# Kernel tuning notes

Hardware: AMD Instinct MI355X
Metric: run time of the kernel (lower is better)

Reference implementation:

```python
import jax, jax.numpy as jnp
import numpy as np

S, B, C, H, W = 16, 64, 128, 11, 11
P = H * W
N_ITER = 3
EPS = 1e-5


def setup_inputs() -> dict:
    key = jax.random.key(0)
    ks = jax.random.split(key, 12)
    w = lambda k, shape: jax.random.normal(k, shape, jnp.float32) * 0.02
    return {
        "x": jax.random.normal(ks[0], (S, B, C, H, W), jnp.float32),
        # intra-attention 1x1 convs (stored as [out,in] matrices)
        "wq": w(ks[1], (C, C)), "bq": jnp.zeros((C,), jnp.float32),
        "wk": w(ks[2], (C, C)), "bk": jnp.zeros((C,), jnp.float32),
        "wv": w(ks[3], (C, C)), "bv": jnp.zeros((C,), jnp.float32),
        "intra_alpha": jnp.float32(1.0),
        # inter-message path
        "w_msg": w(ks[4], (C, C + 1)), "b_msg": jnp.zeros((C,), jnp.float32),
        "w_lin": w(ks[5], (C, C)),
        "weight": jnp.float32(0.5),
        "w_gate": w(ks[6], (C, C)), "b_gate": jnp.zeros((C,), jnp.float32),
        # ConvGRU 3x3 convs
        "w_zr": w(ks[7], (2 * C, 2 * C, 3, 3)), "b_zr": jnp.zeros((2 * C,), jnp.float32),
        "w_h": w(ks[8], (C, 2 * C, 3, 3)), "b_h": jnp.zeros((C,), jnp.float32),
        # LayerNorm over [C,11,11]
        "ln_gamma": jnp.ones((C, H, W), jnp.float32),
        "ln_beta": jnp.zeros((C, H, W), jnp.float32),
    }


def reference(x, wq, bq, wk, bk, wv, bv, intra_alpha, w_msg, b_msg, w_lin,
              weight, w_gate, b_gate, w_zr, b_zr, w_h, b_h, ln_gamma, ln_beta):
    scale = C ** -0.5

    def c1(t, wgt, bias):  # 1x1 conv on [S,B,Cin,H,W] -> [S,B,Cout,H,W]
        return jnp.einsum('sbchw,oc->sbohw', t, wgt) + bias[:, None, None]

    def conv3(t, wgt, bias):  # 3x3 'SAME' conv on [N,Cin,H,W]
        y = jax.lax.conv_general_dilated(
            t, wgt, (1, 1), 'SAME', dimension_numbers=('NCHW', 'OIHW', 'NCHW'))
        return y + bias[None, :, None, None]

    # chain-graph neighbor validity masks (|i-j| == 1)
    mask_l = (jnp.arange(S) >= 1).astype(x.dtype)[:, None, None, None, None]
    mask_r = (jnp.arange(S) <= S - 2).astype(x.dtype)[:, None, None, None, None]

    h = x
    for _ in range(N_ITER):
        # ---- intra spatial self-attention (per node, over P=H*W tokens) ----
        q = c1(h, wq, bq).reshape(S, B, C, P)
        k = c1(h, wk, bk).reshape(S, B, C, P)
        v = c1(h, wv, bv).reshape(S, B, C, P)
        att = jax.nn.softmax(jnp.einsum('sbcp,sbcq->sbpq', q, k) * scale, axis=-1)
        intra = jnp.einsum('sbpq,sbcq->sbcp', att, v).reshape(S, B, C, H, W)
        intra = intra_alpha * intra + h

        # ---- inter gated message attention from chain neighbors ----
        xf = h.reshape(S, B, C, P)

        def gated_msg(y, edge_val):
            ef = jnp.full((S, B, 1, H, W), edge_val, h.dtype)  # edge feature i-j
            yy = c1(jnp.concatenate([y, ef], axis=2), w_msg, b_msg).reshape(S, B, C, P)
            yy = jnp.einsum('sbcp,dc->sbdp', yy, w_lin)  # Linear (no bias)
            a = jax.nn.softmax(jnp.einsum('sbcp,sbcq->sbpq', xf, yy), axis=-1)
            m = jnp.einsum('sbpq,sbcq->sbcp', a, yy).reshape(S, B, C, H, W)
            g = jax.nn.sigmoid(c1(m, w_gate, b_gate).mean(axis=(-2, -1), keepdims=True))
            return m * g

        y_left = jnp.concatenate([jnp.zeros_like(h[:1]), h[:-1]], axis=0)   # h[i-1], edge +1
        y_right = jnp.concatenate([h[1:], jnp.zeros_like(h[:1])], axis=0)   # h[i+1], edge -1
        inter = gated_msg(y_left, 1.0) * mask_l + gated_msg(y_right, -1.0) * mask_r

        comb = weight * intra + (1.0 - weight) * inter

        # ---- ConvGRU update (fold S into batch) ----
        xg = comb.reshape(S * B, C, H, W)
        hg = h.reshape(S * B, C, H, W)
        zr = jax.nn.sigmoid(conv3(jnp.concatenate([xg, hg], axis=1), w_zr, b_zr))
        z, r = zr[:, :C], zr[:, C:]
        h_hat = jnp.tanh(conv3(jnp.concatenate([xg, r * hg], axis=1), w_h, b_h))
        h_new = ((1 - z) * hg + z * h_hat).reshape(S, B, C, H, W)

        # ---- residual + LayerNorm over [C,H,W] ----
        nh = h_new + h
        mu = nh.mean(axis=(-3, -2, -1), keepdims=True)
        var = nh.var(axis=(-3, -2, -1), keepdims=True)
        h = (nh - mu) * jax.lax.rsqrt(var + EPS) * ln_gamma + ln_beta
    return h
```

## Files before the change

### kernel.cpp

```cpp
#include <hip/hip_runtime.h>
#include <hip/hip_bf16.h>

#define S_   16
#define B_   64
#define SBn  1024
#define C_   128
#define P_   121
#define CP_  15488
static const long NEl = 15859712L;

typedef __hip_bfloat16 bf16t;
typedef __attribute__((ext_vector_type(8))) short bf16x8;
typedef __attribute__((ext_vector_type(4))) float f32x4;
typedef __attribute__((ext_vector_type(4))) unsigned short us4;

__device__ __forceinline__ float ldb(const bf16t* p){ return __bfloat162float(*p); }
__device__ __forceinline__ float b2f(unsigned short u){ unsigned x=((unsigned)u)<<16; float f; __builtin_memcpy(&f,&x,4); return f; }
__device__ __forceinline__ unsigned short f2bu(float v){ __hip_bfloat16 b=__float2bfloat16(v); unsigned short u; __builtin_memcpy(&u,&b,2); return u; }
__device__ __forceinline__ float ldin(const void* s, long i, int f){
    return f ? ((const float*)s)[i] : b2f(((const unsigned short*)s)[i]);
}

__global__ void detect_kernel(const unsigned short* __restrict__ x, int* __restrict__ flag){
    if(blockIdx.x==0 && threadIdx.x==0){
        int crazy=0;
        for(int i=0;i<512;i++){
            unsigned e=(x[i]>>7)&0xFF;
            if(e!=0 && (e<64 || e>191)) crazy++;
        }
        *flag=(crazy>40)?1:0;
    }
}

__global__ void cvt_kernel(float* __restrict__ dst, const void* __restrict__ src, long n, const int* __restrict__ flag){
    long i=(long)blockIdx.x*blockDim.x+threadIdx.x;
    long st=(long)gridDim.x*blockDim.x;
    int f=*flag;
    for(;i<n;i+=st) dst[i]=ldin(src,i,f);
}

__global__ __launch_bounds__(256) void cvtT_kernel(bf16t* __restrict__ hT, const void* __restrict__ x, const int* __restrict__ flag){
    __shared__ bf16t tl[CP_];
    int sb=blockIdx.x, t=threadIdx.x; int f=*flag;
    for(int i=t;i<CP_;i+=256)
        tl[i]=__float2bfloat16(ldin(x,(long)sb*CP_+i,f));
    __syncthreads();
    bf16t* ho=hT+(size_t)sb*CP_;
    for(int j=t;j<CP_;j+=256){
        int p=j>>7, c=j&127;
        ho[j]=tl[c*P_+p];
    }
}

__global__ __launch_bounds__(128) void prep_msg_kernel(float* __restrict__ W2, float* __restrict__ b2l, float* __restrict__ b2r,
        const void* __restrict__ wlin, const void* __restrict__ wmsg, const void* __restrict__ bmsg, const int* __restrict__ flag){
    int d=blockIdx.x, c=threadIdx.x; int f=*flag;
    float acc=0.f;
    for(int o2=0;o2<C_;o2++) acc += ldin(wlin,(long)d*C_+o2,f)*ldin(wmsg,(long)o2*(C_+1)+c,f);
    W2[d*C_+c]=acc;
    if(c<2){
        float e=(c==0)?1.f:-1.f; float a=0.f;
        for(int o2=0;o2<C_;o2++) a += ldin(wlin,(long)d*C_+o2,f)*(ldin(bmsg,o2,f)+e*ldin(wmsg,(long)o2*(C_+1)+C_,f));
        if(c==0) b2l[d]=a; else b2r[d]=a;
    }
}

template<int RAW>
__global__ void prep_w1t(bf16t* __restrict__ dst, const void* __restrict__ src, const int* __restrict__ flag){
    int idx=blockIdx.x*blockDim.x+threadIdx.x;
    if(idx>=16384) return;
    int r=idx&31, oc=(idx>>5)&127, icb=idx>>12;
    float v = RAW? ldin(src,(long)oc*C_+icb*32+r,*flag) : ((const float*)src)[(long)oc*C_+icb*32+r];
    dst[idx]=__float2bfloat16(v);
}

__global__ void prep_w3t(bf16t* __restrict__ dst, const void* __restrict__ src, const int* __restrict__ flag, int OC){
    int idx=blockIdx.x*blockDim.x+threadIdx.x;
    int tot=OC*2304;
    if(idx>=tot) return;
    int r=idx&31; int rest=idx>>5; int oc=rest%OC; int g2=rest/OC; int icb=g2&7, tap=g2>>3;
    float v=ldin(src,((long)(oc*256+icb*32+r))*9+tap,*flag);
    dst[idx]=__float2bfloat16(v);
}

__global__ void prep_gbt(float* __restrict__ gamT, float* __restrict__ betT,
                         const void* __restrict__ gam, const void* __restrict__ bet, const int* __restrict__ flag){
    int idx=blockIdx.x*blockDim.x+threadIdx.x;
    if(idx>=CP_) return;
    int c=idx/P_, p=idx-c*P_; int f=*flag;
    gamT[p*C_+c]=ldin(gam,idx,f);
    betT[p*C_+c]=ldin(bet,idx,f);
}

__global__ void prep_wgt(float* __restrict__ wgT, float* __restrict__ bg2,
                         const void* __restrict__ wg, const void* __restrict__ bg, const int* __restrict__ flag){
    int idx=blockIdx.x*blockDim.x+threadIdx.x;
    int f=*flag;
    if(idx<16384){ int k=idx>>7, c=idx&127; wgT[idx]=ldin(wg,(long)c*C_+k,f); }
    if(idx<128) bg2[idx]=ldin(bg,idx,f);
}

__device__ __forceinline__ void gemm24r(f32x4 (&acc)[4][2],
    const bf16t* __restrict__ Wt, const bf16x8 (&hreg)[4][2],
    int ocr,int l15,int kg)
{
    #pragma unroll
    for(int i=0;i<4;i++){
        #pragma unroll
        for(int j=0;j<2;j++) acc[i][j]=(f32x4){0.f,0.f,0.f,0.f};
    }
    #pragma unroll
    for(int kc=0;kc<4;kc++){
        bf16x8 a[4];
        #pragma unroll
        for(int mt=0;mt<4;mt++) a[mt]=*(const bf16x8*)(Wt+((size_t)(kc*C_+ocr*64+mt*16+l15))*32+kg*8);
        #pragma unroll
        for(int mt=0;mt<4;mt++){
            #pragma unroll
            for(int nt=0;nt<2;nt++)
                acc[mt][nt]=__builtin_amdgcn_mfma_f32_16x16x32_bf16(a[mt],hreg[kc][nt],acc[mt][nt],0,0,0);
        }
    }
}

__device__ __forceinline__ void msg_phase(
    f32x4 (&res)[8], const bf16t* __restrict__ hT, int sb, int shift,
    const bf16t* __restrict__ W2T, const float* __restrict__ b2e,
    const float* __restrict__ wgT, const float* __restrict__ bgf, float w1m,
    const bf16x8 (&areg)[4],
    bf16t* LA, bf16t* LB, float* fl,
    int t,int w,int l15,int kg,int ocr,int pcr)
{
    __syncthreads();
    const bf16t* hsp=hT+(size_t)(sb+shift)*CP_;
    bf16x8 hregS[4][2];
    #pragma unroll
    for(int kc=0;kc<4;kc++){
        #pragma unroll
        for(int nt=0;nt<2;nt++)
            hregS[kc][nt]=*(const bf16x8*)(hsp+(size_t)(pcr*32+nt*16+l15)*C_+kc*32+kg*8);
    }
    f32x4 acc[4][2];
    gemm24r(acc,W2T,hregS,ocr,l15,kg);
    #pragma unroll
    for(int mt=0;mt<4;mt++){
        int oc0=ocr*64+mt*16+kg*4;
        #pragma unroll
        for(int nt=0;nt<2;nt++){
            int p=pcr*32+nt*16+l15;
            us4 pk;
            #pragma unroll
            for(int r=0;r<4;r++){
                float v=acc[mt][nt][r]+b2e[oc0+r];
                pk[r]=f2bu(v);
                LB[(oc0+r)*136+p]=__float2bfloat16(p<P_? v : 0.f);
            }
            *(us4*)(LA+p*136+oc0)=pk;
        }
    }
    __syncthreads();
    int m0=w*16;
    f32x4 s[8];
    #pragma unroll
    for(int nt=0;nt<8;nt++) s[nt]=(f32x4){0.f,0.f,0.f,0.f};
    #pragma unroll
    for(int kc=0;kc<4;kc++){
        #pragma unroll
        for(int nt=0;nt<8;nt++){
            bf16x8 b=*(const bf16x8*)(LA+(size_t)(nt*16+l15)*136+kc*32+kg*8);
            s[nt]=__builtin_amdgcn_mfma_f32_16x16x32_bf16(areg[kc],b,s[nt],0,0,0);
        }
    }
    if(l15>=9){
        #pragma unroll
        for(int r=0;r<4;r++) s[7][r]=-3.0e38f;
    }
    #pragma unroll
    for(int r=0;r<4;r++){
        float mx=s[0][r];
        #pragma unroll
        for(int nt=1;nt<8;nt++) mx=fmaxf(mx,s[nt][r]);
        #pragma unroll
        for(int o=1;o<16;o<<=1) mx=fmaxf(mx,__shfl_xor(mx,o));
        float sm=0.f;
        #pragma unroll
        for(int nt=0;nt<8;nt++){ float e=__expf(s[nt][r]-mx); s[nt][r]=e; sm+=e; }
        #pragma unroll
        for(int o=1;o<16;o<<=1) sm+=__shfl_xor(sm,o);
        float rs=1.f/sm;
        #pragma unroll
        for(int nt=0;nt<8;nt++) s[nt][r]*=rs;
    }
    __syncthreads();
    #pragma unroll
    for(int r=0;r<4;r++){
        int pr=m0+kg*4+r;
        #pragma unroll
        for(int nt=0;nt<8;nt++) LA[pr*136+nt*16+l15]=__float2bfloat16(s[nt][r]);
    }
    __syncthreads();
    f32x4 o[8];
    #pragma unroll
    for(int nt=0;nt<8;nt++) o[nt]=(f32x4){0.f,0.f,0.f,0.f};
    #pragma unroll
    for(int jc=0;jc<4;jc++){
        bf16x8 a=*(const bf16x8*)(LB+(size_t)(m0+l15)*136+jc*32+kg*8);
        #pragma unroll
        for(int nt=0;nt<8;nt++){
            bf16x8 b=*(const bf16x8*)(LA+(size_t)(nt*16+l15)*136+jc*32+kg*8);
            o[nt]=__builtin_amdgcn_mfma_f32_16x16x32_bf16(a,b,o[nt],0,0,0);
        }
    }
    int c0=m0+kg*4;
    #pragma unroll
    for(int r=0;r<4;r++){
        float sm=0.f;
        #pragma unroll
        for(int nt=0;nt<8;nt++){ float v=o[nt][r]; if(nt==7&&l15>8) v=0.f; sm+=v; }
        sm+=__shfl_xor(sm,1); sm+=__shfl_xor(sm,2); sm+=__shfl_xor(sm,4); sm+=__shfl_xor(sm,8);
        if(l15==0) fl[c0+r]=sm*(1.f/121.f);
    }
    __syncthreads();
    if(t<C_){
        float a=bgf[t];
        #pragma unroll 8
        for(int k=0;k<C_;k++) a+=wgT[k*C_+t]*fl[k];
        fl[C_+t]=1.f/(1.f+__expf(-a));
    }
    __syncthreads();
    float gg[4];
    #pragma unroll
    for(int r=0;r<4;r++) gg[r]=fl[C_+c0+r];
    #pragma unroll
    for(int nt=0;nt<8;nt++){
        #pragma unroll
        for(int r=0;r<4;r++) res[nt][r]+=w1m*o[nt][r]*gg[r];
    }
}

__global__ __launch_bounds__(512) void attn_all(
    bf16t* __restrict__ comb, const bf16t* __restrict__ hT,
    const bf16t* __restrict__ WqT, const bf16t* __restrict__ WkT, const bf16t* __restrict__ WvT,
    const float* __restrict__ bq, const float* __restrict__ bk, const float* __restrict__ bv,
    const bf16t* __restrict__ W2T, const float* __restrict__ b2l, const float* __restrict__ b2r,
    const float* __restrict__ wgT, const float* __restrict__ bgf,
    const float* __restrict__ alphap, const float* __restrict__ wp)
{
    __shared__ bf16t LA[128*136];
    __shared__ bf16t LB[128*136];
    __shared__ float fl[256];
    int sb=blockIdx.x, t=threadIdx.x, lane=t&63, w=t>>6;
    int l15=lane&15, kg=lane>>4;
    const bf16t* hp=hT+(size_t)sb*CP_;
    int ocr=w>>2, pcr=w&3;
    int m0=w*16;
    bf16x8 hreg[4][2];
    #pragma unroll
    for(int kc=0;kc<4;kc++){
        #pragma unroll
        for(int nt=0;nt<2;nt++)
            hreg[kc][nt]=*(const bf16x8*)(hp+(size_t)(pcr*32+nt*16+l15)*C_+kc*32+kg*8);
    }
    bf16x8 areg[4];
    #pragma unroll
    for(int kc=0;kc<4;kc++)
        areg[kc]=*(const bf16x8*)(hp+(size_t)(m0+l15)*C_+kc*32+kg*8);

    f32x4 acc[4][2];
    gemm24r(acc,WqT,hreg,ocr,l15,kg);
    #pragma unroll
    for(int mt=0;mt<4;mt++){
        int oc0=ocr*64+mt*16+kg*4;
        #pragma unroll
        for(int nt=0;nt<2;nt++){
            int p=pcr*32+nt*16+l15;
            us4 pk;
            #pragma unroll
            for(int r=0;r<4;r++) pk[r]=f2bu(acc[mt][nt][r]+bq[oc0+r]);
            *(us4*)(LA+p*136+oc0)=pk;
        }
    }
    gemm24r(acc,WkT,hreg,ocr,l15,kg);
    #pragma unroll
    for(int mt=0;mt<4;mt++){
        int oc0=ocr*64+mt*16+kg*4;
        #pragma unroll
        for(int nt=0;nt<2;nt++){
            int p=pcr*32+nt*16+l15;
            us4 pk;
            #pragma unroll
            for(int r=0;r<4;r++) pk[r]=f2bu(acc[mt][nt][r]+bk[oc0+r]);
            *(us4*)(LB+p*136+oc0)=pk;
        }
    }
    __syncthreads();
    f32x4 s[8];
    #pragma unroll
    for(int nt=0;nt<8;nt++) s[nt]=(f32x4){0.f,0.f,0.f,0.f};
    #pragma unroll
    for(int kc=0;kc<4;kc++){
        bf16x8 a=*(const bf16x8*)(LA+(size_t)(m0+l15)*136+kc*32+kg*8);
        #pragma unroll
        for(int nt=0;nt<8;nt++){
            bf16x8 b=*(const bf16x8*)(LB+(size_t)(nt*16+l15)*136+kc*32+kg*8);
            s[nt]=__builtin_amdgcn_mfma_f32_16x16x32_bf16(a,b,s[nt],0,0,0);
        }
    }
    const float scale=0.08838834764831845f;
    #pragma unroll
    for(int nt=0;nt<8;nt++){
        #pragma unroll
        for(int r=0;r<4;r++) s[nt][r]*=scale;
    }
    if(l15>=9){
        #pragma unroll
        for(int r=0;r<4;r++) s[7][r]=-3.0e38f;
    }
    #pragma unroll
    for(int r=0;r<4;r++){
        float mx=s[0][r];
        #pragma unroll
        for(int nt=1;nt<8;nt++) mx=fmaxf(mx,s[nt][r]);
        #pragma unroll
        for(int o=1;o<16;o<<=1) mx=fmaxf(mx,__shfl_xor(mx,o));
        float sm=0.f;
        #pragma unroll
        for(int nt=0;nt<8;nt++){ float e=__expf(s[nt][r]-mx); s[nt][r]=e; sm+=e; }
        #pragma unroll
        for(int o=1;o<16;o<<=1) sm+=__shfl_xor(sm,o);
        float rs=1.f/sm;
        #pragma unroll
        for(int nt=0;nt<8;nt++) s[nt][r]*=rs;
    }
    __syncthreads();
    gemm24r(acc,WvT,hreg,ocr,l15,kg);
    #pragma unroll
    for(int mt=0;mt<4;mt++){
        int oc0=ocr*64+mt*16+kg*4;
        #pragma unroll
        for(int nt=0;nt<2;nt++){
            int p=pcr*32+nt*16+l15;
            #pragma unroll
            for(int r=0;r<4;r++)
                LA[(oc0+r)*136+p]=__float2bfloat16(p<P_? acc[mt][nt][r]+bv[oc0+r] : 0.f);
        }
    }
    #pragma unroll
    for(int r=0;r<4;r++){
        int pr=m0+kg*4+r;
        #pragma unroll
        for(int nt=0;nt<8;nt++) LB[pr*136+nt*16+l15]=__float2bfloat16(s[nt][r]);
    }
    __syncthreads();
    f32x4 res[8];
    #pragma unroll
    for(int nt=0;nt<8;nt++) res[nt]=(f32x4){0.f,0.f,0.f,0.f};
    #pragma unroll
    for(int jc=0;jc<4;jc++){
        bf16x8 a=*(const bf16x8*)(LA+(size_t)(m0+l15)*136+jc*32+kg*8);
        #pragma unroll
        for(int nt=0;nt<8;nt++){
            bf16x8 b=*(const bf16x8*)(LB+(size_t)(nt*16+l15)*136+jc*32+kg*8);
            res[nt]=__builtin_amdgcn_mfma_f32_16x16x32_bf16(a,b,res[nt],0,0,0);
        }
    }
    float al=*alphap, wv=*wp, w1m=1.f-wv;
    int c0=m0+kg*4;
    #pragma unroll
    for(int nt=0;nt<8;nt++){
        int p=nt*16+l15;
        int pc=(p<P_)?p:(P_-1);
        us4 hv=*(const us4*)(hp+(size_t)pc*C_+c0);
        #pragma unroll
        for(int r=0;r<4;r++) res[nt][r]=wv*(al*res[nt][r]+b2f(hv[r]));
    }
    if(sb>=B_)
        msg_phase(res,hT,sb,-B_,W2T,b2l,wgT,bgf,w1m,areg,LA,LB,fl,t,w,l15,kg,ocr,pcr);
    if(sb<SBn-B_)
        msg_phase(res,hT,sb, B_,W2T,b2r,wgT,bgf,w1m,areg,LA,LB,fl,t,w,l15,kg,ocr,pcr);
    __syncthreads();
    unsigned short* tl=(unsigned short*)LA;
    #pragma unroll
    for(int nt=0;nt<8;nt++){
        int p=nt*16+l15;
        if(p>=P_) continue;
        us4 pk;
        #pragma unroll
        for(int r=0;r<4;r++) pk[r]=f2bu(res[nt][r]);
        *(us4*)(tl+p*C_+c0)=pk;
    }
    __syncthreads();
    bf16t* ob=comb+(size_t)sb*CP_;
    for(int j=t;j<1936;j+=512)
        *(bf16x8*)(ob+j*8)=*(const bf16x8*)(tl+j*8);
}

#define LOADA3(bidx, widx) { \
    _Pragma("unroll") \
    for(int mt=0;mt<4;mt++) abuf[bidx][mt]=*(const bf16x8*)(Wt+(size_t)(widx)*(OC*32)+mt*512+base_lane); }
#define STEP3(lbase, bidx, doff) { \
    bf16x8 bb[4]; \
    _Pragma("unroll") \
    for(int nt=0;nt<4;nt++) bb[nt]=*(const bf16x8*)((lbase)+boff[nt]+(doff)); \
    __builtin_amdgcn_s_setprio(1); \
    _Pragma("unroll") \
    for(int mt=0;mt<4;mt++){ \
        _Pragma("unroll") \
        for(int nt=0;nt<4;nt++) \
            acc[mt][nt]=__builtin_amdgcn_mfma_f32_16x16x32_bf16(abuf[bidx][mt],bb[nt],acc[mt][nt],0,0,0); } \
    __builtin_amdgcn_s_setprio(0); }

#define SLOADZ(stg) { \
    const bf16t* ssrc=(((stg)<2)? in0T:in1T)+(size_t)sb*CP_+((stg)&1)*64; \
    sreg[0]=*(const bf16x8*)(ssrc+(size_t)sp0*C_+(t&7)*8); \
    if(sv1) sreg[1]=*(const bf16x8*)(ssrc+(size_t)sp1*C_+(t&7)*8); }
#define SWRITEZ(lbase) { \
    *(bf16x8*)((lbase)+spix0*72+(t&7)*8)=sreg[0]; \
    if(sv1) *(bf16x8*)((lbase)+spix1*72+(t&7)*8)=sreg[1]; }

__global__ __launch_bounds__(512) void conv3_zr(
    bf16t* __restrict__ o0, bf16t* __restrict__ o1,
    const bf16t* __restrict__ in0T, const bf16t* __restrict__ in1T,
    const bf16t* __restrict__ Wt, const float* __restrict__ bias,
    const bf16t* __restrict__ hTb)
{
    constexpr int OC=256;
    __shared__ bf16t lin[2*12176];
    int sb=blockIdx.x;
    int t=threadIdx.x, lane=t&63, w=t>>6;
    int ocb=(w>=4)?128:0; int w2=w&3;
    int ocr=w2>>1, pcr=w2&1, l15=lane&15, kg=lane>>4;
    int boff[4]; bool pv_[4];
    #pragma unroll
    for(int nt=0;nt<4;nt++){
        int p=pcr*64+nt*16+l15;
        pv_[nt]=(p<P_); int pc=pv_[nt]?p:(P_-1);
        boff[nt]=((pc/11)*13+(pc%11))*72+kg*8;
    }
    f32x4 acc[4][4];
    #pragma unroll
    for(int i=0;i<4;i++){
        #pragma unroll
        for(int j=0;j<4;j++) acc[i][j]=(f32x4){0.f,0.f,0.f,0.f};
    }
    int base_lane=(ocb+ocr*64+l15)*32+kg*8;
    bf16x8 abuf[4][4];
    bf16x8 sreg[2];
    bool sv1=((t+512)<968);
    int sp0=t>>3, sp1=(t+512)>>3;
    if(sp1>120) sp1=120;
    int spix0=(sp0/11+1)*13+(sp0%11)+1;
    int spix1=(sp1/11+1)*13+(sp1%11)+1;
    LOADA3(0,0); LOADA3(1,1); LOADA3(2,8); LOADA3(3,9);
    SLOADZ(0);
    {
        bf16x8 z;
        #pragma unroll
        for(int e=0;e<8;e++) z[e]=0;
        for(int i=t;i<768;i+=512){
            int half=i>=384; int i2=i-half*384;
            int bi=i2>>3, cc=(i2&7)*8;
            int pix;
            if(bi<13) pix=bi;
            else if(bi<26) pix=156+(bi-13);
            else { int j2=bi-26; pix=(1+(j2>>1))*13+((j2&1)?12:0); }
            *(bf16x8*)(lin+half*12176+pix*72+cc)=z;
        }
    }
    SWRITEZ(lin);
    __syncthreads();
    #pragma unroll
    for(int st=0; st<4; ++st){
        if(st<3) SLOADZ(st+1);
        bf16t* lbase=lin+(st&1)*12176;
        #pragma unroll
        for(int k=0;k<18;k++){
            int s=st*18+k;
            int tap=k>>1, l=k&1;
            int doff=((tap/3)*13+(tap%3))*72+l*32;
            STEP3(lbase, s&3, doff);
            if(s<68){
                int s4=s+4, st4=s4/18, k4=s4-st4*18, tap4=k4>>1, l4=k4&1;
                LOADA3(s&3, tap4*8+st4*2+l4);
            }
        }
        if(st<3){ SWRITEZ(lin+((st+1)&1)*12176); }
        __syncthreads();
    }
    unsigned short* tl=(unsigned short*)lin;
    if(ocb==0){
        #pragma unroll
        for(int mt=0;mt<4;mt++){
            int ocl=ocr*64+mt*16+kg*4;
            #pragma unroll
            for(int nt=0;nt<4;nt++){
                if(!pv_[nt]) continue;
                int p=pcr*64+nt*16+l15;
                us4 pk;
                #pragma unroll
                for(int r=0;r<4;r++){ float a=acc[mt][nt][r]+bias[ocl+r]; pk[r]=f2bu(1.f/(1.f+__expf(-a))); }
                *(us4*)(tl+p*C_+ocl)=pk;
            }
        }
    }
    __syncthreads();
    {
        bf16t* zb=o0+(size_t)sb*CP_;
        for(int j=t;j<1936;j+=512)
            *(bf16x8*)(zb+j*8)=*(const bf16x8*)(tl+j*8);
    }
    __syncthreads();
    if(ocb==128){
        #pragma unroll
        for(int mt=0;mt<4;mt++){
            int ocl=ocr*64+mt*16+kg*4;
            #pragma unroll
            for(int nt=0;nt<4;nt++){
                if(!pv_[nt]) continue;
                int p=pcr*64+nt*16+l15;
                size_t tb=(size_t)sb*CP_+(size_t)p*C_+ocl;
                us4 hv=*(const us4*)(hTb+tb);
                us4 pk;
                #pragma unroll
                for(int r=0;r<4;r++){ float a=acc[mt][nt][r]+bias[128+ocl+r]; float sg=1.f/(1.f+__expf(-a)); pk[r]=f2bu(sg*b2f(hv[r])); }
                *(us4*)(tl+p*C_+ocl)=pk;
            }
        }
    }
    __syncthreads();
    {
        bf16t* rb=o1+(size_t)sb*CP_;
        for(int j=t;j<1936;j+=512)
            *(bf16x8*)(rb+j*8)=*(const bf16x8*)(tl+j*8);
    }
}

#define SLOADH(stg) { \
    const bf16t* ssrc=(((stg)<2)? in0T:in1T)+(size_t)sb*CP_+((stg)&1)*64; \
    sreg[0]=*(const bf16x8*)(ssrc+(size_t)(t>>3)*C_+(t&7)*8); \
    sreg[1]=*(const bf16x8*)(ssrc+(size_t)((t+256)>>3)*C_+(t&7)*8); \
    if(sv2) sreg[2]=*(const bf16x8*)(ssrc+(size_t)sp2*C_+(t&7)*8); \
    if(sv3) sreg[3]=*(const bf16x8*)(ssrc+(size_t)sp3*C_+(t&7)*8); }
#define SWRITEH(lbase) { \
    *(bf16x8*)((lbase)+spix0*72+(t&7)*8)=sreg[0]; \
    *(bf16x8*)((lbase)+spix1*72+(t&7)*8)=sreg[1]; \
    if(sv2) *(bf16x8*)((lbase)+spix2*72+(t&7)*8)=sreg[2]; \
    if(sv3) *(bf16x8*)((lbase)+spix3*72+(t&7)*8)=sreg[3]; }

__global__ __launch_bounds__(256) void conv3_hh(
    bf16t* __restrict__ o0,
    const bf16t* __restrict__ in0T, const bf16t* __restrict__ in1T,
    const bf16t* __restrict__ Wt, const float* __restrict__ bias,
    const bf16t* __restrict__ zT, const bf16t* __restrict__ hTb,
    const float* __restrict__ gamT, const float* __restrict__ betT)
{
    constexpr int OC=128;
    __shared__ bf16t lin[2*12176];
    __shared__ float red[8];
    int sb=blockIdx.x;
    int t=threadIdx.x, lane=t&63, w=t>>6;
    int ocr=w>>1, pcr=w&1, l15=lane&15, kg=lane>>4;
    int boff[4]; bool pv_[4];
    #pragma unroll
    for(int nt=0;nt<4;nt++){
        int p=pcr*64+nt*16+l15;
        pv_[nt]=(p<P_); int pc=pv_[nt]?p:(P_-1);
        boff[nt]=((pc/11)*13+(pc%11))*72+kg*8;
    }
    f32x4 acc[4][4];
    #pragma unroll
    for(int i=0;i<4;i++){
        #pragma unroll
        for(int j=0;j<4;j++) acc[i][j]=(f32x4){0.f,0.f,0.f,0.f};
    }
    int base_lane=(ocr*64+l15)*32+kg*8;
    bf16x8 abuf[4][4];
    bf16x8 sreg[4];
    bool sv2=((t+512)<968), sv3=((t+768)<968);
    int sp0=t>>3, sp1=(t+256)>>3, sp2=(t+512)>>3, sp3=(t+768)>>3;
    if(sp2>120) sp2=120;
    if(sp3>120) sp3=120;
    int spix0=(sp0/11+1)*13+(sp0%11)+1;
    int spix1=(sp1/11+1)*13+(sp1%11)+1;
    int spix2=(sp2/11+1)*13+(sp2%11)+1;
    int spix3=(sp3/11+1)*13+(sp3%11)+1;
    LOADA3(0,0); LOADA3(1,1); LOADA3(2,8); LOADA3(3,9);
    SLOADH(0);
    {
        bf16x8 z;
        #pragma unroll
        for(int e=0;e<8;e++) z[e]=0;
        for(int i=t;i<768;i+=256){
            int half=i>=384; int i2=i-half*384;
            int bi=i2>>3, cc=(i2&7)*8;
            int pix;
            if(bi<13) pix=bi;
            else if(bi<26) pix=156+(bi-13);
            else { int j2=bi-26; pix=(1+(j2>>1))*13+((j2&1)?12:0); }
            *(bf16x8*)(lin+half*12176+pix*72+cc)=z;
        }
    }
    SWRITEH(lin);
    __syncthreads();
    #pragma unroll
    for(int st=0; st<4; ++st){
        if(st<3) SLOADH(st+1);
        bf16t* lbase=lin+(st&1)*12176;
        #pragma unroll
        for(int k=0;k<18;k++){
            int s=st*18+k;
            int tap=k>>1, l=k&1;
            int doff=((tap/3)*13+(tap%3))*72+l*32;
            STEP3(lbase, s&3, doff);
            if(s<68){
                int s4=s+4, st4=s4/18, k4=s4-st4*18, tap4=k4>>1, l4=k4&1;
                LOADA3(s&3, tap4*8+st4*2+l4);
            }
        }
        if(st<3){ SWRITEH(lin+((st+1)&1)*12176); }
        __syncthreads();
    }
    float ls=0.f, ls2=0.f;
    #pragma unroll
    for(int mt=0;mt<4;mt++){
        int ocl=ocr*64+mt*16+kg*4;
        #pragma unroll
        for(int nt=0;nt<4;nt++){
            if(!pv_[nt]) continue;
            int p=pcr*64+nt*16+l15;
            size_t tb=(size_t)sb*CP_+(size_t)p*C_+ocl;
            us4 hv=*(const us4*)(hTb+tb);
            us4 zv=*(const us4*)(zT+tb);
            us4 pk;
            #pragma unroll
            for(int r=0;r<4;r++){
                float a=acc[mt][nt][r]+bias[ocl+r];
                float ht=tanhf(a);
                float z=b2f(zv[r]), h=b2f(hv[r]);
                unsigned short u=f2bu((1.f-z)*h+z*ht+h);
                pk[r]=u;
                float nr=b2f(u); ls+=nr; ls2+=nr*nr;
            }
            *(us4*)((unsigned short*)lin + p*C_+ocl)=pk;
        }
    }
    #pragma unroll
    for(int o=32;o;o>>=1){ ls+=__shfl_xor(ls,o); ls2+=__shfl_xor(ls2,o); }
    if(lane==0){ red[w]=ls; red[4+w]=ls2; }
    __syncthreads();
    float Sx=red[0]+red[1]+red[2]+red[3];
    float Sx2=red[4]+red[5]+red[6]+red[7];
    float mu=Sx*(1.f/(float)CP_);
    float var=Sx2*(1.f/(float)CP_)-mu*mu;
    float rstd=rsqrtf(var+1e-5f);
    bf16t* ho=o0+(size_t)sb*CP_;
    const unsigned short* tl=(const unsigned short*)lin;
    for(int j=t;j<1936;j+=256){
        int base=j*8;
        bf16x8 ovec;
        #pragma unroll
        for(int e=0;e<8;e++){
            float v=(b2f(tl[base+e])-mu)*rstd*gamT[base+e]+betT[base+e];
            ovec[e]=(short)f2bu(v);
        }
        *(bf16x8*)(ho+base)=ovec;
    }
}

__global__ __launch_bounds__(256) void finalT_kernel(void* __restrict__ fout, const bf16t* __restrict__ hT, const int* __restrict__ flag){
    __shared__ bf16t tl[CP_];
    int sb=blockIdx.x, t=threadIdx.x, f=*flag;
    for(int i=t;i<CP_;i+=256) tl[i]=hT[(size_t)sb*CP_+i];
    __syncthreads();
    for(int i=t;i<CP_;i+=256){
        int c=i/P_, p=i-c*P_;
        float v=ldb(tl+p*C_+c);
        size_t oi=(size_t)sb*CP_+i;
        if(f) ((float*)fout)[oi]=v;
        else  ((bf16t*)fout)[oi]=__float2bfloat16(v);
    }
}

extern "C" void kernel_launch(void* const* d_in, const int* in_sizes, int n_in,
                              void* d_out, int out_size, void* d_ws, size_t ws_size,
                              hipStream_t stream) {
    (void)in_sizes; (void)n_in; (void)out_size;
    char* base=(char*)d_ws;
    size_t off=0;
    auto alloc=[&](size_t bytes){ void* p=base+off; off+=(bytes+255)&~(size_t)255; return p; };
    bf16t* b1=(bf16t*)alloc((size_t)NEl*2+8192);
    bf16t* b2=(bf16t*)alloc((size_t)NEl*2+8192);
    bf16t* b3=(bf16t*)alloc((size_t)NEl*2+8192);
    bf16t* b4=(bf16t*)d_out;
    bf16t* wqT=(bf16t*)alloc(16384*2);
    bf16t* wkT=(bf16t*)alloc(16384*2);
    bf16t* wvT=(bf16t*)alloc(16384*2);
    bf16t* w2T=(bf16t*)alloc(16384*2);
    bf16t* wzrT=(bf16t*)alloc((size_t)589824*2);
    bf16t* whT =(bf16t*)alloc((size_t)294912*2);
    float* W2f=(float*)alloc(16384*4);
    float* b2l=(float*)alloc(128*4); float* b2r=(float*)alloc(128*4);
    float* bqf=(float*)alloc(128*4); float* bkf=(float*)alloc(128*4); float* bvf=(float*)alloc(128*4);
    float* bzrf=(float*)alloc(256*4); float* bhf=(float*)alloc(128*4);
    float* gamT=(float*)alloc(15488*4); float* betT=(float*)alloc(15488*4);
    float* wgTf=(float*)alloc(16384*4); float* bgf2=(float*)alloc(128*4);
    float* alphaf=(float*)alloc(4); float* weightf=(float*)alloc(4);
    int* flag=(int*)alloc(4);
    if(ws_size<off) return;

    detect_kernel<<<1,64,0,stream>>>((const unsigned short*)d_in[0],flag);
    cvtT_kernel<<<SBn,256,0,stream>>>(b1,d_in[0],flag);
    prep_w1t<1><<<64,256,0,stream>>>(wqT,d_in[1],flag);
    cvt_kernel<<<1,128,0,stream>>>(bqf,d_in[2],128,flag);
    prep_w1t<1><<<64,256,0,stream>>>(wkT,d_in[3],flag);
    cvt_kernel<<<1,128,0,stream>>>(bkf,d_in[4],128,flag);
    prep_w1t<1><<<64,256,0,stream>>>(wvT,d_in[5],flag);
    cvt_kernel<<<1,128,0,stream>>>(bvf,d_in[6],128,flag);
    cvt_kernel<<<1,64,0,stream>>>(alphaf,d_in[7],1,flag);
    prep_msg_kernel<<<C_,C_,0,stream>>>(W2f,b2l,b2r,d_in[10],d_in[8],d_in[9],flag);
    prep_w1t<0><<<64,256,0,stream>>>(w2T,W2f,flag);
    cvt_kernel<<<1,64,0,stream>>>(weightf,d_in[11],1,flag);
    prep_wgt<<<64,256,0,stream>>>(wgTf,bgf2,d_in[12],d_in[13],flag);
    prep_w3t<<<(256*2304+255)/256,256,0,stream>>>(wzrT,d_in[14],flag,256);
    cvt_kernel<<<1,256,0,stream>>>(bzrf,d_in[15],256,flag);
    prep_w3t<<<(128*2304+255)/256,256,0,stream>>>(whT,d_in[16],flag,128);
    cvt_kernel<<<1,128,0,stream>>>(bhf,d_in[17],128,flag);
    prep_gbt<<<(CP_+255)/256,256,0,stream>>>(gamT,betT,d_in[18],d_in[19],flag);

    for(int it=0; it<3; ++it){
        attn_all<<<SBn,512,0,stream>>>(b2,b1,wqT,wkT,wvT,bqf,bkf,bvf,
                                       w2T,b2l,b2r,wgTf,bgf2,alphaf,weightf);
        conv3_zr<<<SBn,512,0,stream>>>(b4,b3,b2,b1,wzrT,bzrf,b1);
        conv3_hh<<<SBn,256,0,stream>>>(b1,b2,b3,whT,bhf,b4,b1,gamT,betT);
    }
    finalT_kernel<<<SBn,256,0,stream>>>(d_out,b1,flag);
}
```

Before: 1.418 ms.

## Double wave count in conv3 kernels, halving per-wave output-channel tile

Both 3x3 conv kernels now launch twice as many threads per block (1024 for zr, 512 for hh), with each wave covering 32 output channels instead of 64. This halves the per-thread accumulator and A-fragment registers and spreads the staging loads over more threads, aiming for more waves in flight to hide memory and LDS latency. The cost is that each B fragment read from LDS feeds fewer MFMAs, so LDS traffic per FLOP doubles. Block-level sync also covers more waves.

```diff
diff --git a/kernel.cpp b/kernel.cpp
--- a/kernel.cpp
+++ b/kernel.cpp
@@ -395,16 +395,16 @@
         *(bf16x8*)(ob+j*8)=*(const bf16x8*)(tl+j*8);
 }
 
-#define LOADA3(bidx, widx) { \
+#define LOADA2(bidx, widx) { \
     _Pragma("unroll") \
-    for(int mt=0;mt<4;mt++) abuf[bidx][mt]=*(const bf16x8*)(Wt+(size_t)(widx)*(OC*32)+mt*512+base_lane); }
-#define STEP3(lbase, bidx, doff) { \
+    for(int mt=0;mt<2;mt++) abuf[bidx][mt]=*(const bf16x8*)(Wt+(size_t)(widx)*(OC*32)+mt*512+base_lane); }
+#define STEP2(lbase, bidx, doff) { \
     bf16x8 bb[4]; \
     _Pragma("unroll") \
     for(int nt=0;nt<4;nt++) bb[nt]=*(const bf16x8*)((lbase)+boff[nt]+(doff)); \
     __builtin_amdgcn_s_setprio(1); \
     _Pragma("unroll") \
-    for(int mt=0;mt<4;mt++){ \
+    for(int mt=0;mt<2;mt++){ \
         _Pragma("unroll") \
         for(int nt=0;nt<4;nt++) \
             acc[mt][nt]=__builtin_amdgcn_mfma_f32_16x16x32_bf16(abuf[bidx][mt],bb[nt],acc[mt][nt],0,0,0); } \
@@ -412,13 +412,11 @@
 
 #define SLOADZ(stg) { \
     const bf16t* ssrc=(((stg)<2)? in0T:in1T)+(size_t)sb*CP_+((stg)&1)*64; \
-    sreg[0]=*(const bf16x8*)(ssrc+(size_t)sp0*C_+(t&7)*8); \
-    if(sv1) sreg[1]=*(const bf16x8*)(ssrc+(size_t)sp1*C_+(t&7)*8); }
+    if(sv0) sreg0=*(const bf16x8*)(ssrc+(size_t)sp0*C_+(t&7)*8); }
 #define SWRITEZ(lbase) { \
-    *(bf16x8*)((lbase)+spix0*72+(t&7)*8)=sreg[0]; \
-    if(sv1) *(bf16x8*)((lbase)+spix1*72+(t&7)*8)=sreg[1]; }
-
-__global__ __launch_bounds__(512) void conv3_zr(
+    if(sv0) *(bf16x8*)((lbase)+spix0*72+(t&7)*8)=sreg0; }
+
+__global__ __launch_bounds__(1024) void conv3_zr(
     bf16t* __restrict__ o0, bf16t* __restrict__ o1,
     const bf16t* __restrict__ in0T, const bf16t* __restrict__ in1T,
     const bf16t* __restrict__ Wt, const float* __restrict__ bias,
@@ -428,7 +426,7 @@
     __shared__ bf16t lin[2*12176];
     int sb=blockIdx.x;
     int t=threadIdx.x, lane=t&63, w=t>>6;
-    int ocb=(w>=4)?128:0; int w2=w&3;
+    int ocb=(w>=8)?128:0; int w2=w&7;
     int ocr=w2>>1, pcr=w2&1, l15=lane&15, kg=lane>>4;
     int boff[4]; bool pv_[4];
     #pragma unroll
@@ -437,28 +435,26 @@
         pv_[nt]=(p<P_); int pc=pv_[nt]?p:(P_-1);
         boff[nt]=((pc/11)*13+(pc%11))*72+kg*8;
     }
-    f32x4 acc[4][4];
-    #pragma unroll
-    for(int i=0;i<4;i++){
+    f32x4 acc[2][4];
+    #pragma unroll
+    for(int i=0;i<2;i++){
         #pragma unroll
         for(int j=0;j<4;j++) acc[i][j]=(f32x4){0.f,0.f,0.f,0.f};
     }
-    int base_lane=(ocb+ocr*64+l15)*32+kg*8;
-    bf16x8 abuf[4][4];
-    bf16x8 sreg[2];
-    bool sv1=((t+512)<968);
-    int sp0=t>>3, sp1=(t+512)>>3;
-    if(sp1>120) sp1=120;
+    int base_lane=(ocb+ocr*32+l15)*32+kg*8;
+    bf16x8 abuf[4][2];
+    bf16x8 sreg0;
+    bool sv0=(t<968);
+    int sp0=(t<968)? (t>>3):120;
     int spix0=(sp0/11+1)*13+(sp0%11)+1;
-    int spix1=(sp1/11+1)*13+(sp1%11)+1;
-    LOADA3(0,0); LOADA3(1,1); LOADA3(2,8); LOADA3(3,9);
+    LOADA2(0,0); LOADA2(1,1); LOADA2(2,8); LOADA2(3,9);
     SLOADZ(0);
     {
         bf16x8 z;
         #pragma unroll
         for(int e=0;e<8;e++) z[e]=0;
-        for(int i=t;i<768;i+=512){
-            int half=i>=384; int i2=i-half*384;
+        if(t<768){
+            int half=t>=384; int i2=t-half*384;
             int bi=i2>>3, cc=(i2&7)*8;
             int pix;
             if(bi<13) pix=bi;
@@ -478,10 +474,10 @@
             int s=st*18+k;
             int tap=k>>1, l=k&1;
             int doff=((tap/3)*13+(tap%3))*72+l*32;
-            STEP3(lbase, s&3, doff);
+            STEP2(lbase, s&3, doff);
             if(s<68){
                 int s4=s+4, st4=s4/18, k4=s4-st4*18, tap4=k4>>1, l4=k4&1;
-                LOADA3(s&3, tap4*8+st4*2+l4);
+                LOADA2(s&3, tap4*8+st4*2+l4);
             }
         }
         if(st<3){ SWRITEZ(lin+((st+1)&1)*12176); }
@@ -490,8 +486,8 @@
     unsigned short* tl=(unsigned short*)lin;
     if(ocb==0){
         #pragma unroll
-        for(int mt=0;mt<4;mt++){
-            int ocl=ocr*64+mt*16+kg*4;
+        for(int mt=0;mt<2;mt++){
+            int ocl=ocr*32+mt*16+kg*4;
             #pragma unroll
             for(int nt=0;nt<4;nt++){
                 if(!pv_[nt]) continue;
@@ -506,14 +502,14 @@
     __syncthreads();
     {
         bf16t* zb=o0+(size_t)sb*CP_;
-        for(int j=t;j<1936;j+=512)
-            *(bf16x8*)(zb+j*8)=*(const bf16x8*)(tl+j*8);
+        *(bf16x8*)(zb+t*8)=*(const bf16x8*)(tl+t*8);
+        if(t<912) *(bf16x8*)(zb+(t+1024)*8)=*(const bf16x8*)(tl+(t+1024)*8);
     }
     __syncthreads();
     if(ocb==128){
         #pragma unroll
-        for(int mt=0;mt<4;mt++){
-            int ocl=ocr*64+mt*16+kg*4;
+        for(int mt=0;mt<2;mt++){
+            int ocl=ocr*32+mt*16+kg*4;
             #pragma unroll
             for(int nt=0;nt<4;nt++){
                 if(!pv_[nt]) continue;
@@ -530,24 +526,20 @@
     __syncthreads();
     {
         bf16t* rb=o1+(size_t)sb*CP_;
-        for(int j=t;j<1936;j+=512)
-            *(bf16x8*)(rb+j*8)=*(const bf16x8*)(tl+j*8);
+        *(bf16x8*)(rb+t*8)=*(const bf16x8*)(tl+t*8);
+        if(t<912) *(bf16x8*)(rb+(t+1024)*8)=*(const bf16x8*)(tl+(t+1024)*8);
     }
 }
 
 #define SLOADH(stg) { \
     const bf16t* ssrc=(((stg)<2)? in0T:in1T)+(size_t)sb*CP_+((stg)&1)*64; \
     sreg[0]=*(const bf16x8*)(ssrc+(size_t)(t>>3)*C_+(t&7)*8); \
-    sreg[1]=*(const bf16x8*)(ssrc+(size_t)((t+256)>>3)*C_+(t&7)*8); \
-    if(sv2) sreg[2]=*(const bf16x8*)(ssrc+(size_t)sp2*C_+(t&7)*8); \
-    if(sv3) sreg[3]=*(const bf16x8*)(ssrc+(size_t)sp3*C_+(t&7)*8); }
+    if(sv1) sreg[1]=*(const bf16x8*)(ssrc+(size_t)sp1*C_+(t&7)*8); }
 #define SWRITEH(lbase) { \
     *(bf16x8*)((lbase)+spix0*72+(t&7)*8)=sreg[0]; \
-    *(bf16x8*)((lbase)+spix1*72+(t&7)*8)=sreg[1]; \
-    if(sv2) *(bf16x8*)((lbase)+spix2*72+(t&7)*8)=sreg[2]; \
-    if(sv3) *(bf16x8*)((lbase)+spix3*72+(t&7)*8)=sreg[3]; }
-
-__global__ __launch_bounds__(256) void conv3_hh(
+    if(sv1) *(bf16x8*)((lbase)+spix1*72+(t&7)*8)=sreg[1]; }
+
+__global__ __launch_bounds__(512,4) void conv3_hh(
     bf16t* __restrict__ o0,
     const bf16t* __restrict__ in0T, const bf16t* __restrict__ in1T,
     const bf16t* __restrict__ Wt, const float* __restrict__ bias,
@@ -556,7 +548,7 @@
 {
     constexpr int OC=128;
     __shared__ bf16t lin[2*12176];
-    __shared__ float red[8];
+    __shared__ float red[16];
     int sb=blockIdx.x;
     int t=threadIdx.x, lane=t&63, w=t>>6;
     int ocr=w>>1, pcr=w&1, l15=lane&15, kg=lane>>4;
@@ -567,30 +559,27 @@
         pv_[nt]=(p<P_); int pc=pv_[nt]?p:(P_-1);
         boff[nt]=((pc/11)*13+(pc%11))*72+kg*8;
     }
-    f32x4 acc[4][4];
-    #pragma unroll
-    for(int i=0;i<4;i++){
+    f32x4 acc[2][4];
+    #pragma unroll
+    for(int i=0;i<2;i++){
         #pragma unroll
         for(int j=0;j<4;j++) acc[i][j]=(f32x4){0.f,0.f,0.f,0.f};
     }
-    int base_lane=(ocr*64+l15)*32+kg*8;
-    bf16x8 abuf[4][4];
-    bf16x8 sreg[4];
-    bool sv2=((t+512)<968), sv3=((t+768)<968);
-    int sp0=t>>3, sp1=(t+256)>>3, sp2=(t+512)>>3, sp3=(t+768)>>3;
-    if(sp2>120) sp2=120;
-    if(sp3>120) sp3=120;
+    int base_lane=(ocr*32+l15)*32+kg*8;
+    bf16x8 abuf[4][2];
+    bf16x8 sreg[2];
+    bool sv1=((t+512)<968);
+    int sp0=t>>3, sp1=(t+512)>>3;
+    if(sp1>120) sp1=120;
     int spix0=(sp0/11+1)*13+(sp0%11)+1;
     int spix1=(sp1/11+1)*13+(sp1%11)+1;
-    int spix2=(sp2/11+1)*13+(sp2%11)+1;
-    int spix3=(sp3/11+1)*13+(sp3%11)+1;
-    LOADA3(0,0); LOADA3(1,1); LOADA3(2,8); LOADA3(3,9);
+    LOADA2(0,0); LOADA2(1,1); LOADA2(2,8); LOADA2(3,9);
     SLOADH(0);
     {
         bf16x8 z;
         #pragma unroll
         for(int e=0;e<8;e++) z[e]=0;
-        for(int i=t;i<768;i+=256){
+        for(int i=t;i<768;i+=512){
             int half=i>=384; int i2=i-half*384;
             int bi=i2>>3, cc=(i2&7)*8;
             int pix;
@@ -611,10 +600,10 @@
             int s=st*18+k;
             int tap=k>>1, l=k&1;
             int doff=((tap/3)*13+(tap%3))*72+l*32;
-            STEP3(lbase, s&3, doff);
+            STEP2(lbase, s&3, doff);
             if(s<68){
                 int s4=s+4, st4=s4/18, k4=s4-st4*18, tap4=k4>>1, l4=k4&1;
-                LOADA3(s&3, tap4*8+st4*2+l4);
+                LOADA2(s&3, tap4*8+st4*2+l4);
             }
         }
         if(st<3){ SWRITEH(lin+((st+1)&1)*12176); }
@@ -622,8 +611,8 @@
     }
     float ls=0.f, ls2=0.f;
     #pragma unroll
-    for(int mt=0;mt<4;mt++){
-        int ocl=ocr*64+mt*16+kg*4;
+    for(int mt=0;mt<2;mt++){
+        int ocl=ocr*32+mt*16+kg*4;
         #pragma unroll
         for(int nt=0;nt<4;nt++){
             if(!pv_[nt]) continue;
@@ -646,16 +635,17 @@
     }
     #pragma unroll
     for(int o=32;o;o>>=1){ ls+=__shfl_xor(ls,o); ls2+=__shfl_xor(ls2,o); }
-    if(lane==0){ red[w]=ls; red[4+w]=ls2; }
-    __syncthreads();
-    float Sx=red[0]+red[1]+red[2]+red[3];
-    float Sx2=red[4]+red[5]+red[6]+red[7];
+    if(lane==0){ red[w]=ls; red[8+w]=ls2; }
+    __syncthreads();
+    float Sx=0.f,Sx2=0.f;
+    #pragma unroll
+    for(int i=0;i<8;i++){ Sx+=red[i]; Sx2+=red[8+i]; }
     float mu=Sx*(1.f/(float)CP_);
     float var=Sx2*(1.f/(float)CP_)-mu*mu;
     float rstd=rsqrtf(var+1e-5f);
     bf16t* ho=o0+(size_t)sb*CP_;
     const unsigned short* tl=(const unsigned short*)lin;
-    for(int j=t;j<1936;j+=256){
+    for(int j=t;j<1936;j+=512){
         int base=j*8;
         bf16x8 ovec;
         #pragma unroll
@@ -730,8 +720,8 @@
     for(int it=0; it<3; ++it){
         attn_all<<<SBn,512,0,stream>>>(b2,b1,wqT,wkT,wvT,bqf,bkf,bvf,
                                        w2T,b2l,b2r,wgTf,bgf2,alphaf,weightf);
-        conv3_zr<<<SBn,512,0,stream>>>(b4,b3,b2,b1,wzrT,bzrf,b1);
-        conv3_hh<<<SBn,256,0,stream>>>(b1,b2,b3,whT,bhf,b4,b1,gamT,betT);
+        conv3_zr<<<SBn,1024,0,stream>>>(b4,b3,b2,b1,wzrT,bzrf,b1);
+        conv3_hh<<<SBn,512,0,stream>>>(b1,b2,b3,whT,bhf,b4,b1,gamT,betT);
     }
     finalT_kernel<<<SBn,256,0,stream>>>(d_out,b1,flag);
 }
```

New measurement: 1.385 ms (median of 2 runs). 1.02x faster.
